# Performance work log

Measured on AMD Instinct MI355X. Metric: run time of the kernel, lower is better.

## Reference

```python
import jax, jax.numpy as jnp
import numpy as np

D_MODEL, D_K, D_V, H = 1024, 64, 64, 16
B, NQ, NK = 2, 2048, 2048


def setup_inputs() -> dict:
    key = jax.random.key(0)
    ks = jax.random.split(key, 12)
    hd = H * D_K
    xav = lambda k, shape: jax.random.uniform(k, shape, jnp.float32, -1.0, 1.0) * np.sqrt(6.0 / (shape[0] + shape[1]))
    return {
        "queries": jax.random.normal(ks[0], (B, NQ, D_MODEL), jnp.float32),
        "keys": jax.random.normal(ks[1], (B, NK, D_MODEL), jnp.float32),
        "values": jax.random.normal(ks[2], (B, NK, D_MODEL), jnp.float32),
        "memory": jax.random.uniform(ks[3], (B, NK), jnp.float32),
        "Wq": xav(ks[4], (D_MODEL, hd)), "bq": jnp.zeros((hd,), jnp.float32),
        "Wk": xav(ks[5], (D_MODEL, hd)), "bk": jnp.zeros((hd,), jnp.float32),
        "Wv": xav(ks[6], (D_MODEL, H * D_V)), "bv": jnp.zeros((H * D_V,), jnp.float32),
        "Wo": xav(ks[7], (H * D_V, D_MODEL)), "bo": jnp.zeros((D_MODEL,), jnp.float32),
        "Wmm": xav(ks[8], (1, H * D_V)), "bmm": jnp.zeros((H * D_V,), jnp.float32),
    }


def reference(queries, keys, values, memory, Wq, bq, Wk, bk, Wv, bv, Wo, bo, Wmm, bmm):
    b, nq = queries.shape[:2]
    nk = keys.shape[1]
    # projections -> (b, h, n, d)
    q = (queries @ Wq + bq).reshape(b, nq, H, D_K).transpose(0, 2, 1, 3)
    k = (keys @ Wk + bk).reshape(b, nk, H, D_K).transpose(0, 2, 1, 3)
    v = (values @ Wv + bv).reshape(b, nk, H, D_V).transpose(0, 2, 1, 3)
    # memory gate: fc_mm(memory[..., None]) -> (b, nk, h*d_k) -> (b, h, nk, d_k)
    mm = (memory[:, :, None] * Wmm[0] + bmm).reshape(b, nk, H, D_K).transpose(0, 2, 1, 3)
    att = jnp.einsum("bhqd,bhkd->bhqk", q, k * mm) / np.sqrt(D_K).astype(np.float32)
    att = jax.nn.softmax(att, axis=-1)
    out = jnp.einsum("bhqk,bhkd->bhqd", att, v * mm)
    out = out.transpose(0, 2, 1, 3).reshape(b, nq, H * D_V)
    return out @ Wo + bo
```

## Files before the change

### kernel.cpp

```cpp
#include <hip/hip_runtime.h>
#include <hip/hip_bf16.h>

#define H_   16
#define NQ_  2048
#define NK_  2048
#define DM_  1024

typedef float f32x4 __attribute__((ext_vector_type(4)));
typedef __bf16 bf16x8 __attribute__((ext_vector_type(8)));
typedef unsigned short u16x8 __attribute__((ext_vector_type(8)));

__device__ __forceinline__ unsigned short bfbits(float x) {
  __bf16 h = (__bf16)x;
  return __builtin_bit_cast(unsigned short, h);
}

__global__ __launch_bounds__(256) void transpose_cvt4(
    const float* __restrict__ s0, const float* __restrict__ s1,
    const float* __restrict__ s2, const float* __restrict__ s3,
    unsigned short* __restrict__ d0, unsigned short* __restrict__ d1,
    unsigned short* __restrict__ d2, unsigned short* __restrict__ d3) {
  const float* src = (blockIdx.z == 0) ? s0 : (blockIdx.z == 1) ? s1 : (blockIdx.z == 2) ? s2 : s3;
  unsigned short* dst = (blockIdx.z == 0) ? d0 : (blockIdx.z == 1) ? d1 : (blockIdx.z == 2) ? d2 : d3;
  __shared__ float t[64][65];
  const int r0 = blockIdx.x * 64, c0 = blockIdx.y * 64;
  for (int i = threadIdx.x; i < 4096; i += 256) {
    int r = i >> 6, c = i & 63;
    t[r][c] = src[(size_t)(r0 + r) * DM_ + c0 + c];
  }
  __syncthreads();
  for (int i = threadIdx.x; i < 4096; i += 256) {
    int n = i >> 6, k = i & 63;
    dst[(size_t)(c0 + n) * DM_ + r0 + k] = bfbits(t[k][n]);
  }
}

__device__ __forceinline__ void gll16(const unsigned short* g, unsigned short* l) {
  __builtin_amdgcn_global_load_lds((const __attribute__((address_space(1))) void*)g,
                                   (__attribute__((address_space(3))) void*)l, 16, 0, 0);
}

template <int MODE>
__device__ __forceinline__ void gemm_body(
    int bx, int by,
    const void* __restrict__ Av, const void* __restrict__ Btv, int K,
    const float* __restrict__ bias, const float* __restrict__ mem,
    const float* __restrict__ Wmm, const float* __restrict__ bmm,
    unsigned short* __restrict__ obf, float* __restrict__ of32,
    unsigned short* Al, unsigned short* Bl) {
  constexpr bool AF32 = (MODE <= 1);
  constexpr bool BF32 = (MODE == 2);
  const int tid = threadIdx.x, lane = tid & 63, w = tid >> 6;
  const int wm = w >> 1, wn = w & 1;
  const int m0 = bx * 64, n0 = by * 128;
  const int lrow = lane >> 2, lcol = (lane & 3) * 8;
  const int fr = lane & 15, fk = (lane >> 4) * 8;

  f32x4 acc[2][4] = {};

  const size_t aoff = (size_t)(m0 + w * 16 + lrow) * K + lcol;
  const size_t boff = (size_t)(n0 + w * 32 + lrow) * K + lcol;
  const unsigned short* ag = (const unsigned short*)Av + aoff;
  const float*          agf = (const float*)Av + aoff;
  const unsigned short* bg = (const unsigned short*)Btv + boff;
  const float*          bgf = (const float*)Btv + boff;
  unsigned short* la0 = &Al[(w * 16) * 32];
  unsigned short* lawr = &Al[(w * 16 + lrow) * 32 + lcol];
  unsigned short* lb0 = &Bl[(w * 32) * 32];
  unsigned short* lb1 = &Bl[(w * 32 + 16) * 32];
  unsigned short* lbwr0 = &Bl[(w * 32 + lrow) * 32 + lcol];
  unsigned short* lbwr1 = &Bl[(w * 32 + 16 + lrow) * 32 + lcol];
  const size_t s16K = (size_t)16 * K;

  const int KT = K >> 5;
  for (int kt = 0; kt < KT; ++kt) {
    if constexpr (AF32) {
      float4 x0 = *(const float4*)agf;
      float4 x1 = *(const float4*)(agf + 4);
      agf += 32;
      bf16x8 o;
      o[0] = (__bf16)x0.x; o[1] = (__bf16)x0.y; o[2] = (__bf16)x0.z; o[3] = (__bf16)x0.w;
      o[4] = (__bf16)x1.x; o[5] = (__bf16)x1.y; o[6] = (__bf16)x1.z; o[7] = (__bf16)x1.w;
      *(bf16x8*)lawr = o;
    } else {
      gll16(ag, la0);
      ag += 32;
    }
    if constexpr (BF32) {
      float4 y0 = *(const float4*)bgf;
      float4 y1 = *(const float4*)(bgf + 4);
      float4 y2 = *(const float4*)(bgf + s16K);
      float4 y3 = *(const float4*)(bgf + s16K + 4);
      bgf += 32;
      bf16x8 o0, o1;
      o0[0] = (__bf16)y0.x; o0[1] = (__bf16)y0.y; o0[2] = (__bf16)y0.z; o0[3] = (__bf16)y0.w;
      o0[4] = (__bf16)y1.x; o0[5] = (__bf16)y1.y; o0[6] = (__bf16)y1.z; o0[7] = (__bf16)y1.w;
      o1[0] = (__bf16)y2.x; o1[1] = (__bf16)y2.y; o1[2] = (__bf16)y2.z; o1[3] = (__bf16)y2.w;
      o1[4] = (__bf16)y3.x; o1[5] = (__bf16)y3.y; o1[6] = (__bf16)y3.z; o1[7] = (__bf16)y3.w;
      *(bf16x8*)lbwr0 = o0;
      *(bf16x8*)lbwr1 = o1;
    } else {
      gll16(bg, lb0);
      gll16(bg + s16K, lb1);
      bg += 32;
    }
    __syncthreads();
    bf16x8 af[2], bfr[4];
#pragma unroll
    for (int i = 0; i < 2; ++i) af[i] = *(const bf16x8*)&Al[(wm * 32 + i * 16 + fr) * 32 + fk];
#pragma unroll
    for (int j = 0; j < 4; ++j) bfr[j] = *(const bf16x8*)&Bl[(wn * 64 + j * 16 + fr) * 32 + fk];
#pragma unroll
    for (int i = 0; i < 2; ++i)
#pragma unroll
      for (int j = 0; j < 4; ++j)
        acc[i][j] = __builtin_amdgcn_mfma_f32_16x16x32_bf16(af[i], bfr[j], acc[i][j], 0, 0, 0);
    __syncthreads();
  }

#pragma unroll
  for (int i = 0; i < 2; ++i) {
    const int rowb = m0 + wm * 32 + i * 16 + (lane >> 4) * 4;
#pragma unroll
    for (int j = 0; j < 4; ++j) {
      const int col = n0 + wn * 64 + j * 16 + fr;
#pragma unroll
      for (int r = 0; r < 4; ++r) {
        float v = acc[i][j][r];
        int rr = rowb + r;
        if (MODE == 0) {
          int b = rr >> 11, nq = rr & 2047, h = col >> 6, d = col & 63;
          float val = (v + bias[col]) * 0.180336884f;
          obf[(((size_t)(b * H_ + h)) * NQ_ + nq) * 64 + d] = bfbits(val);
        } else if (MODE == 1) {
          int b = rr >> 11, nk = rr & 2047, h = col >> 6, d = col & 63;
          float gate = mem[b * NK_ + nk] * Wmm[col] + bmm[col];
          float val = (v + bias[col]) * gate;
          obf[(((size_t)(b * H_ + h)) * NK_ + nk) * 64 + d] = bfbits(val);
        } else if (MODE == 2) {
          int b = col >> 11, key = col & 2047, h = rr >> 6, d = rr & 63;
          float gate = mem[b * NK_ + key] * Wmm[rr] + bmm[rr];
          float val = (v + bias[rr]) * gate;
          int keyp = (key & ~31) | ((key & 12) << 1) | ((key & 16) >> 2) | (key & 3);
          obf[(((size_t)(b * H_ + h)) * 64 + d) * NK_ + keyp] = bfbits(val);
        } else {
          of32[(size_t)rr * DM_ + col] = v + bias[col];
        }
      }
    }
  }
}

__global__ __launch_bounds__(256) void gemm_qkv(
    const float* __restrict__ queries, const float* __restrict__ keys,
    const unsigned short* __restrict__ WvT, const float* __restrict__ values,
    const unsigned short* __restrict__ WqT, const unsigned short* __restrict__ WkT,
    const float* __restrict__ bq, const float* __restrict__ bk, const float* __restrict__ bv,
    const float* __restrict__ mem, const float* __restrict__ Wmm, const float* __restrict__ bmm,
    unsigned short* __restrict__ Qp, unsigned short* __restrict__ Kp,
    unsigned short* __restrict__ VpT) {
  __shared__ unsigned short Al[64 * 32];
  __shared__ unsigned short Bl[128 * 32];
  const int b = (blockIdx.x & 7) * 192 + (blockIdx.x >> 3);
  if (b < 512) {
    gemm_body<0>(b & 63, b >> 6, queries, WqT, 1024, bq, nullptr, nullptr, nullptr,
                 Qp, nullptr, Al, Bl);
  } else if (b < 1024) {
    int bb = b - 512;
    gemm_body<1>(bb & 63, bb >> 6, keys, WkT, 1024, bk, mem, Wmm, bmm, Kp, nullptr, Al, Bl);
  } else {
    int bb = b - 1024;
    gemm_body<2>(bb & 15, bb >> 4, WvT, values, 1024, bv, mem, Wmm, bmm, VpT, nullptr, Al, Bl);
  }
}

__global__ __launch_bounds__(256) void gemm_out(
    const unsigned short* __restrict__ AO, const unsigned short* __restrict__ WoT,
    const float* __restrict__ bo, float* __restrict__ out) {
  __shared__ unsigned short Al[64 * 32];
  __shared__ unsigned short Bl[128 * 32];
  const int b = (blockIdx.x & 7) * 64 + (blockIdx.x >> 3);
  gemm_body<3>(b & 63, b >> 6, AO, WoT, 1024, bo, nullptr, nullptr, nullptr,
               nullptr, out, Al, Bl);
}

__global__ __launch_bounds__(512, 6) void flash_attn(const unsigned short* __restrict__ Qp,
                                                     const unsigned short* __restrict__ Kp,
                                                     const unsigned short* __restrict__ VpT,
                                                     unsigned short* __restrict__ AO) {
  __shared__ unsigned short Ks[2][64][72];
  __shared__ unsigned short Vs[2][64][72];

  const int tid = threadIdx.x, lane = tid & 63, w = tid >> 6;
  const int gid = (blockIdx.x & 7) * 64 + (blockIdx.x >> 3);
  const int bh = gid >> 4;
  const int qt = gid & 15;
  const int fr = lane & 15, hi = lane >> 4, fk8 = hi * 8;
  const int w16 = w * 16;

  const unsigned short* qg = Qp + (((size_t)bh * NQ_) + qt * 128 + w16 + fr) * 64;
  bf16x8 aq0 = *(const bf16x8*)&qg[fk8];
  bf16x8 aq1 = *(const bf16x8*)&qg[32 + fk8];

  const int srow = tid >> 3, scol = (tid & 7) * 8;
  const unsigned short* kg = Kp + ((size_t)bh * NK_ + srow) * 64 + scol;
  const unsigned short* vg = VpT + ((size_t)bh * 64 + srow) * NK_ + scol;

  f32x4 acc_o[4] = {};
  float m_run = -1e30f, l_run = 0.0f;

  {
    u16x8 k0 = *(const u16x8*)kg;
    u16x8 v0 = *(const u16x8*)vg;
    *(u16x8*)&Ks[0][srow][scol] = k0;
    *(u16x8*)&Vs[0][srow][scol] = v0;
  }

  u16x8 kreg, vreg;
  for (int kt = 0; kt < 32; ++kt) {
    const int cur = kt & 1;
    if (kt + 1 < 32) {
      kreg = *(const u16x8*)(kg + (kt + 1) * 64 * 64);
      vreg = *(const u16x8*)(vg + (kt + 1) * 64);
    }
    __syncthreads();

    f32x4 sv[4];
    __builtin_amdgcn_s_setprio(1);
#pragma unroll
    for (int kk = 0; kk < 4; ++kk) {
      bf16x8 b0 = *(const bf16x8*)&Ks[cur][kk * 16 + fr][fk8];
      bf16x8 b1 = *(const bf16x8*)&Ks[cur][kk * 16 + fr][32 + fk8];
      f32x4 z = {0.f, 0.f, 0.f, 0.f};
      z = __builtin_amdgcn_mfma_f32_16x16x32_bf16(b0, aq0, z, 0, 0, 0);
      sv[kk] = __builtin_amdgcn_mfma_f32_16x16x32_bf16(b1, aq1, z, 0, 0, 0);
    }
    __builtin_amdgcn_s_setprio(0);

    float mx = fmaxf(fmaxf(sv[0][0], sv[0][1]), fmaxf(sv[0][2], sv[0][3]));
#pragma unroll
    for (int kk = 1; kk < 4; ++kk)
      mx = fmaxf(mx, fmaxf(fmaxf(sv[kk][0], sv[kk][1]), fmaxf(sv[kk][2], sv[kk][3])));
    mx = fmaxf(mx, __shfl_xor(mx, 16));
    mx = fmaxf(mx, __shfl_xor(mx, 32));

    if (__any(mx > m_run + 8.0f)) {
      float mnew = fmaxf(m_run, mx);
      float sc = __builtin_amdgcn_exp2f(m_run - mnew);
      m_run = mnew;
      l_run *= sc;
#pragma unroll
      for (int r = 0; r < 4; ++r) {
        float scr = __shfl(sc, hi * 4 + r);
#pragma unroll
        for (int n = 0; n < 4; ++n) acc_o[n][r] *= scr;
      }
    }

    float ps = 0.0f;
    bf16x8 pa0, pa1;
#pragma unroll
    for (int kk = 0; kk < 4; ++kk) {
#pragma unroll
      for (int r = 0; r < 4; ++r) {
        float pv = __builtin_amdgcn_exp2f(sv[kk][r] - m_run);
        ps += pv;
        if (kk < 2) pa0[(kk & 1) * 4 + r] = (__bf16)pv;
        else        pa1[(kk & 1) * 4 + r] = (__bf16)pv;
      }
    }
    ps += __shfl_xor(ps, 16);
    ps += __shfl_xor(ps, 32);
    l_run += ps;

    __builtin_amdgcn_s_setprio(1);
#pragma unroll
    for (int ks = 0; ks < 2; ++ks) {
      bf16x8 pa = ks ? pa1 : pa0;
#pragma unroll
      for (int n = 0; n < 4; ++n) {
        bf16x8 vb = *(const bf16x8*)&Vs[cur][n * 16 + fr][ks * 32 + fk8];
        acc_o[n] = __builtin_amdgcn_mfma_f32_16x16x32_bf16(pa, vb, acc_o[n], 0, 0, 0);
      }
    }
    __builtin_amdgcn_s_setprio(0);

    if (kt + 1 < 32) {
      *(u16x8*)&Ks[cur ^ 1][srow][scol] = kreg;
      *(u16x8*)&Vs[cur ^ 1][srow][scol] = vreg;
    }
  }

  const int b = bh >> 4, h = bh & 15;
  float linv[4];
#pragma unroll
  for (int r = 0; r < 4; ++r) linv[r] = 1.0f / __shfl(l_run, hi * 4 + r);
#pragma unroll
  for (int n = 0; n < 4; ++n)
#pragma unroll
    for (int r = 0; r < 4; ++r) {
      float val = acc_o[n][r] * linv[r];
      int qrow = qt * 128 + w16 + hi * 4 + r;
      int col = h * 64 + n * 16 + fr;
      AO[(((size_t)b * NQ_ + qrow) << 10) + col] = bfbits(val);
    }
}

extern "C" void kernel_launch(void* const* d_in, const int* in_sizes, int n_in,
                              void* d_out, int out_size, void* d_ws, size_t ws_size,
                              hipStream_t stream) {
  const float* queries = (const float*)d_in[0];
  const float* keys    = (const float*)d_in[1];
  const float* values  = (const float*)d_in[2];
  const float* memory  = (const float*)d_in[3];
  const float* Wq  = (const float*)d_in[4];
  const float* bq  = (const float*)d_in[5];
  const float* Wk  = (const float*)d_in[6];
  const float* bk  = (const float*)d_in[7];
  const float* Wv  = (const float*)d_in[8];
  const float* bv  = (const float*)d_in[9];
  const float* Wo  = (const float*)d_in[10];
  const float* bo  = (const float*)d_in[11];
  const float* Wmm = (const float*)d_in[12];
  const float* bmm = (const float*)d_in[13];

  char* ws = (char*)d_ws;
  const size_t SZ_X = (size_t)4096 * 1024 * 2;
  const size_t SZ_W = (size_t)1024 * 1024 * 2;
  unsigned short* AO  = (unsigned short*)(ws);
  size_t off = SZ_X;
  unsigned short* WqT = (unsigned short*)(ws + off); off += SZ_W;
  unsigned short* WkT = (unsigned short*)(ws + off); off += SZ_W;
  unsigned short* WvT = (unsigned short*)(ws + off); off += SZ_W;
  unsigned short* WoT = (unsigned short*)(ws + off); off += SZ_W;
  unsigned short* Qp  = (unsigned short*)(ws + off); off += SZ_X;
  unsigned short* Kp  = (unsigned short*)(ws + off); off += SZ_X;
  unsigned short* VpT = (unsigned short*)(ws + off); off += SZ_X;

  transpose_cvt4<<<dim3(16, 16, 4), 256, 0, stream>>>(Wq, Wk, Wv, Wo, WqT, WkT, WvT, WoT);

  gemm_qkv<<<1536, 256, 0, stream>>>(queries, keys, WvT, values, WqT, WkT,
                                     bq, bk, bv, memory, Wmm, bmm, Qp, Kp, VpT);

  flash_attn<<<512, 512, 0, stream>>>(Qp, Kp, VpT, AO);

  gemm_out<<<512, 256, 0, stream>>>(AO, WoT, bo, (float*)d_out);
}
```

Baseline: 144.0 us.

## Pre-convert activations to bf16 and use 128x128 tiles for QKV GEMM

Adds a separate elementwise kernel that converts queries, keys and values to bf16 up front. The QKV projection GEMM can then load both operands with direct global-to-LDS copies and use larger 128x128 tiles, which doubles the work per block and halves the grid. The goal is to remove the per-iteration fp32 load and convert path and to raise operand reuse. In exchange it adds an extra pass over the activations and a larger workspace, and the output GEMM is inlined as its own specialised kernel.

```diff
diff --git a/kernel.cpp b/kernel.cpp
--- a/kernel.cpp
+++ b/kernel.cpp
@@ -13,6 +13,23 @@
 __device__ __forceinline__ unsigned short bfbits(float x) {
   __bf16 h = (__bf16)x;
   return __builtin_bit_cast(unsigned short, h);
+}
+
+__global__ __launch_bounds__(256) void cvt3(const float* __restrict__ q,
+                                            const float* __restrict__ k,
+                                            const float* __restrict__ v,
+                                            unsigned short* __restrict__ qo,
+                                            unsigned short* __restrict__ ko,
+                                            unsigned short* __restrict__ vo) {
+  const float* src = (blockIdx.y == 0) ? q : (blockIdx.y == 1) ? k : v;
+  unsigned short* dst = (blockIdx.y == 0) ? qo : (blockIdx.y == 1) ? ko : vo;
+  int i = blockIdx.x * 256 + threadIdx.x;
+  const float4* s4 = (const float4*)src;
+  float4 a = s4[2 * i], b = s4[2 * i + 1];
+  bf16x8 o;
+  o[0] = (__bf16)a.x; o[1] = (__bf16)a.y; o[2] = (__bf16)a.z; o[3] = (__bf16)a.w;
+  o[4] = (__bf16)b.x; o[5] = (__bf16)b.y; o[6] = (__bf16)b.z; o[7] = (__bf16)b.w;
+  *((bf16x8*)dst + i) = o;
 }
 
 __global__ __launch_bounds__(256) void transpose_cvt4(
@@ -41,77 +58,42 @@
 }
 
 template <int MODE>
-__device__ __forceinline__ void gemm_body(
+__device__ __forceinline__ void gemm128_body(
     int bx, int by,
-    const void* __restrict__ Av, const void* __restrict__ Btv, int K,
+    const unsigned short* __restrict__ A, const unsigned short* __restrict__ Bt, int K,
     const float* __restrict__ bias, const float* __restrict__ mem,
     const float* __restrict__ Wmm, const float* __restrict__ bmm,
-    unsigned short* __restrict__ obf, float* __restrict__ of32,
+    unsigned short* __restrict__ obf,
     unsigned short* Al, unsigned short* Bl) {
-  constexpr bool AF32 = (MODE <= 1);
-  constexpr bool BF32 = (MODE == 2);
   const int tid = threadIdx.x, lane = tid & 63, w = tid >> 6;
   const int wm = w >> 1, wn = w & 1;
-  const int m0 = bx * 64, n0 = by * 128;
+  const int m0 = bx * 128, n0 = by * 128;
   const int lrow = lane >> 2, lcol = (lane & 3) * 8;
   const int fr = lane & 15, fk = (lane >> 4) * 8;
 
-  f32x4 acc[2][4] = {};
-
-  const size_t aoff = (size_t)(m0 + w * 16 + lrow) * K + lcol;
-  const size_t boff = (size_t)(n0 + w * 32 + lrow) * K + lcol;
-  const unsigned short* ag = (const unsigned short*)Av + aoff;
-  const float*          agf = (const float*)Av + aoff;
-  const unsigned short* bg = (const unsigned short*)Btv + boff;
-  const float*          bgf = (const float*)Btv + boff;
-  unsigned short* la0 = &Al[(w * 16) * 32];
-  unsigned short* lawr = &Al[(w * 16 + lrow) * 32 + lcol];
+  f32x4 acc[4][4] = {};
+
+  const unsigned short* ag0 = A + (size_t)(m0 + w * 32 + lrow) * K + lcol;
+  const unsigned short* bg0 = Bt + (size_t)(n0 + w * 32 + lrow) * K + lcol;
+  unsigned short* la0 = &Al[(w * 32) * 32];
+  unsigned short* la1 = &Al[(w * 32 + 16) * 32];
   unsigned short* lb0 = &Bl[(w * 32) * 32];
   unsigned short* lb1 = &Bl[(w * 32 + 16) * 32];
-  unsigned short* lbwr0 = &Bl[(w * 32 + lrow) * 32 + lcol];
-  unsigned short* lbwr1 = &Bl[(w * 32 + 16 + lrow) * 32 + lcol];
   const size_t s16K = (size_t)16 * K;
 
   const int KT = K >> 5;
   for (int kt = 0; kt < KT; ++kt) {
-    if constexpr (AF32) {
-      float4 x0 = *(const float4*)agf;
-      float4 x1 = *(const float4*)(agf + 4);
-      agf += 32;
-      bf16x8 o;
-      o[0] = (__bf16)x0.x; o[1] = (__bf16)x0.y; o[2] = (__bf16)x0.z; o[3] = (__bf16)x0.w;
-      o[4] = (__bf16)x1.x; o[5] = (__bf16)x1.y; o[6] = (__bf16)x1.z; o[7] = (__bf16)x1.w;
-      *(bf16x8*)lawr = o;
-    } else {
-      gll16(ag, la0);
-      ag += 32;
-    }
-    if constexpr (BF32) {
-      float4 y0 = *(const float4*)bgf;
-      float4 y1 = *(const float4*)(bgf + 4);
-      float4 y2 = *(const float4*)(bgf + s16K);
-      float4 y3 = *(const float4*)(bgf + s16K + 4);
-      bgf += 32;
-      bf16x8 o0, o1;
-      o0[0] = (__bf16)y0.x; o0[1] = (__bf16)y0.y; o0[2] = (__bf16)y0.z; o0[3] = (__bf16)y0.w;
-      o0[4] = (__bf16)y1.x; o0[5] = (__bf16)y1.y; o0[6] = (__bf16)y1.z; o0[7] = (__bf16)y1.w;
-      o1[0] = (__bf16)y2.x; o1[1] = (__bf16)y2.y; o1[2] = (__bf16)y2.z; o1[3] = (__bf16)y2.w;
-      o1[4] = (__bf16)y3.x; o1[5] = (__bf16)y3.y; o1[6] = (__bf16)y3.z; o1[7] = (__bf16)y3.w;
-      *(bf16x8*)lbwr0 = o0;
-      *(bf16x8*)lbwr1 = o1;
-    } else {
-      gll16(bg, lb0);
-      gll16(bg + s16K, lb1);
-      bg += 32;
-    }
-    __syncthreads();
-    bf16x8 af[2], bfr[4];
-#pragma unroll
-    for (int i = 0; i < 2; ++i) af[i] = *(const bf16x8*)&Al[(wm * 32 + i * 16 + fr) * 32 + fk];
+    gll16(ag0, la0); gll16(ag0 + s16K, la1);
+    gll16(bg0, lb0); gll16(bg0 + s16K, lb1);
+    ag0 += 32; bg0 += 32;
+    __syncthreads();
+    bf16x8 af[4], bfr[4];
+#pragma unroll
+    for (int i = 0; i < 4; ++i) af[i] = *(const bf16x8*)&Al[(wm * 64 + i * 16 + fr) * 32 + fk];
 #pragma unroll
     for (int j = 0; j < 4; ++j) bfr[j] = *(const bf16x8*)&Bl[(wn * 64 + j * 16 + fr) * 32 + fk];
 #pragma unroll
-    for (int i = 0; i < 2; ++i)
+    for (int i = 0; i < 4; ++i)
 #pragma unroll
       for (int j = 0; j < 4; ++j)
         acc[i][j] = __builtin_amdgcn_mfma_f32_16x16x32_bf16(af[i], bfr[j], acc[i][j], 0, 0, 0);
@@ -119,8 +101,8 @@
   }
 
 #pragma unroll
-  for (int i = 0; i < 2; ++i) {
-    const int rowb = m0 + wm * 32 + i * 16 + (lane >> 4) * 4;
+  for (int i = 0; i < 4; ++i) {
+    const int rowb = m0 + wm * 64 + i * 16 + (lane >> 4) * 4;
 #pragma unroll
     for (int j = 0; j < 4; ++j) {
       const int col = n0 + wn * 64 + j * 16 + fr;
@@ -137,40 +119,38 @@
           float gate = mem[b * NK_ + nk] * Wmm[col] + bmm[col];
           float val = (v + bias[col]) * gate;
           obf[(((size_t)(b * H_ + h)) * NK_ + nk) * 64 + d] = bfbits(val);
-        } else if (MODE == 2) {
+        } else {
           int b = col >> 11, key = col & 2047, h = rr >> 6, d = rr & 63;
           float gate = mem[b * NK_ + key] * Wmm[rr] + bmm[rr];
           float val = (v + bias[rr]) * gate;
           int keyp = (key & ~31) | ((key & 12) << 1) | ((key & 16) >> 2) | (key & 3);
           obf[(((size_t)(b * H_ + h)) * 64 + d) * NK_ + keyp] = bfbits(val);
-        } else {
-          of32[(size_t)rr * DM_ + col] = v + bias[col];
         }
       }
     }
   }
 }
 
-__global__ __launch_bounds__(256) void gemm_qkv(
-    const float* __restrict__ queries, const float* __restrict__ keys,
-    const unsigned short* __restrict__ WvT, const float* __restrict__ values,
+__global__ __launch_bounds__(256) void gemm_qkv3(
+    const unsigned short* __restrict__ qbf, const unsigned short* __restrict__ kbf,
+    const unsigned short* __restrict__ vbf, const unsigned short* __restrict__ WvT,
     const unsigned short* __restrict__ WqT, const unsigned short* __restrict__ WkT,
     const float* __restrict__ bq, const float* __restrict__ bk, const float* __restrict__ bv,
     const float* __restrict__ mem, const float* __restrict__ Wmm, const float* __restrict__ bmm,
     unsigned short* __restrict__ Qp, unsigned short* __restrict__ Kp,
     unsigned short* __restrict__ VpT) {
-  __shared__ unsigned short Al[64 * 32];
+  __shared__ unsigned short Al[128 * 32];
   __shared__ unsigned short Bl[128 * 32];
-  const int b = (blockIdx.x & 7) * 192 + (blockIdx.x >> 3);
-  if (b < 512) {
-    gemm_body<0>(b & 63, b >> 6, queries, WqT, 1024, bq, nullptr, nullptr, nullptr,
-                 Qp, nullptr, Al, Bl);
-  } else if (b < 1024) {
-    int bb = b - 512;
-    gemm_body<1>(bb & 63, bb >> 6, keys, WkT, 1024, bk, mem, Wmm, bmm, Kp, nullptr, Al, Bl);
+  const int gid = (blockIdx.x & 7) * 96 + (blockIdx.x >> 3);
+  if (gid < 256) {
+    gemm128_body<0>(gid & 31, gid >> 5, qbf, WqT, 1024, bq, nullptr, nullptr, nullptr,
+                    Qp, Al, Bl);
+  } else if (gid < 512) {
+    int bb = gid - 256;
+    gemm128_body<1>(bb & 31, bb >> 5, kbf, WkT, 1024, bk, mem, Wmm, bmm, Kp, Al, Bl);
   } else {
-    int bb = b - 1024;
-    gemm_body<2>(bb & 15, bb >> 4, WvT, values, 1024, bv, mem, Wmm, bmm, VpT, nullptr, Al, Bl);
+    int bb = gid - 512;
+    gemm128_body<2>(bb & 7, bb >> 3, WvT, vbf, 1024, bv, mem, Wmm, bmm, VpT, Al, Bl);
   }
 }
 
@@ -180,8 +160,52 @@
   __shared__ unsigned short Al[64 * 32];
   __shared__ unsigned short Bl[128 * 32];
   const int b = (blockIdx.x & 7) * 64 + (blockIdx.x >> 3);
-  gemm_body<3>(b & 63, b >> 6, AO, WoT, 1024, bo, nullptr, nullptr, nullptr,
-               nullptr, out, Al, Bl);
+  const int bx = b & 63, by = b >> 6;
+  const int tid = threadIdx.x, lane = tid & 63, w = tid >> 6;
+  const int wm = w >> 1, wn = w & 1;
+  const int m0 = bx * 64, n0 = by * 128;
+  const int lrow = lane >> 2, lcol = (lane & 3) * 8;
+  const int fr = lane & 15, fk = (lane >> 4) * 8;
+  const int K = 1024;
+
+  f32x4 acc[2][4] = {};
+
+  const unsigned short* ag = AO + (size_t)(m0 + w * 16 + lrow) * K + lcol;
+  const unsigned short* bg = WoT + (size_t)(n0 + w * 32 + lrow) * K + lcol;
+  unsigned short* la0 = &Al[(w * 16) * 32];
+  unsigned short* lb0 = &Bl[(w * 32) * 32];
+  unsigned short* lb1 = &Bl[(w * 32 + 16) * 32];
+  const size_t s16K = (size_t)16 * K;
+
+  for (int kt = 0; kt < 32; ++kt) {
+    gll16(ag, la0);
+    gll16(bg, lb0); gll16(bg + s16K, lb1);
+    ag += 32; bg += 32;
+    __syncthreads();
+    bf16x8 af[2], bfr[4];
+#pragma unroll
+    for (int i = 0; i < 2; ++i) af[i] = *(const bf16x8*)&Al[(wm * 32 + i * 16 + fr) * 32 + fk];
+#pragma unroll
+    for (int j = 0; j < 4; ++j) bfr[j] = *(const bf16x8*)&Bl[(wn * 64 + j * 16 + fr) * 32 + fk];
+#pragma unroll
+    for (int i = 0; i < 2; ++i)
+#pragma unroll
+      for (int j = 0; j < 4; ++j)
+        acc[i][j] = __builtin_amdgcn_mfma_f32_16x16x32_bf16(af[i], bfr[j], acc[i][j], 0, 0, 0);
+    __syncthreads();
+  }
+
+#pragma unroll
+  for (int i = 0; i < 2; ++i) {
+    const int rowb = m0 + wm * 32 + i * 16 + (lane >> 4) * 4;
+#pragma unroll
+    for (int j = 0; j < 4; ++j) {
+      const int col = n0 + wn * 64 + j * 16 + fr;
+#pragma unroll
+      for (int r = 0; r < 4; ++r)
+        out[(size_t)(rowb + r) * DM_ + col] = acc[i][j][r] + bo[col];
+    }
+  }
 }
 
 __global__ __launch_bounds__(512, 6) void flash_attn(const unsigned short* __restrict__ Qp,
@@ -327,8 +351,11 @@
   char* ws = (char*)d_ws;
   const size_t SZ_X = (size_t)4096 * 1024 * 2;
   const size_t SZ_W = (size_t)1024 * 1024 * 2;
+  unsigned short* qbf = (unsigned short*)(ws);
+  unsigned short* kbf = (unsigned short*)(ws + SZ_X);
+  unsigned short* vbf = (unsigned short*)(ws + 2 * SZ_X);
   unsigned short* AO  = (unsigned short*)(ws);
-  size_t off = SZ_X;
+  size_t off = 3 * SZ_X;
   unsigned short* WqT = (unsigned short*)(ws + off); off += SZ_W;
   unsigned short* WkT = (unsigned short*)(ws + off); off += SZ_W;
   unsigned short* WvT = (unsigned short*)(ws + off); off += SZ_W;
@@ -337,9 +364,10 @@
   unsigned short* Kp  = (unsigned short*)(ws + off); off += SZ_X;
   unsigned short* VpT = (unsigned short*)(ws + off); off += SZ_X;
 
+  cvt3<<<dim3(2048, 3), 256, 0, stream>>>(queries, keys, values, qbf, kbf, vbf);
   transpose_cvt4<<<dim3(16, 16, 4), 256, 0, stream>>>(Wq, Wk, Wv, Wo, WqT, WkT, WvT, WoT);
 
-  gemm_qkv<<<1536, 256, 0, stream>>>(queries, keys, WvT, values, WqT, WkT,
+  gemm_qkv3<<<768, 256, 0, stream>>>(qbf, kbf, vbf, WvT, WqT, WkT,
                                      bq, bk, bv, memory, Wmm, bmm, Qp, Kp, VpT);
 
   flash_attn<<<512, 512, 0, stream>>>(Qp, Kp, VpT, AO);
```

New measurement: 144.3 us. Within noise of the previous version (+0.2%).
